# Kernel tuning notes

Measured on AMD Instinct MI355X. Metric: run time of the kernel, lower is better.

## Reference

```python
import jax, jax.numpy as jnp
import numpy as np

BINS = 64
VMIN, VMAX = 0.0, 1.0


def _calc_histogram(x):
    # x: [B, C, H, W] float
    B, C, H, W = x.shape
    x_norm = jnp.clip((x - VMIN) / (VMAX - VMIN), 0.0, 1.0)
    flat = x_norm.reshape(B * C, H * W)
    # torch.histc semantics over [0,1]: bin i = [i/BINS, (i+1)/BINS), last bin closed.
    idx = jnp.clip((flat * BINS).astype(jnp.int32), 0, BINS - 1)  # [B*C, HW]
    row_offset = (jnp.arange(B * C, dtype=jnp.int32) * BINS)[:, None]
    flat_idx = (idx + row_offset).reshape(-1)
    counts = jax.ops.segment_sum(
        jnp.ones(flat_idx.shape, dtype=x.dtype), flat_idx,
        num_segments=B * C * BINS,
    ).reshape(B * C, BINS)
    counts = counts / jnp.clip(counts.sum(axis=1, keepdims=True), 1e-8, None)
    return counts.reshape(B, C, BINS)


def reference(fake_images, real_images):
    hist_fake = _calc_histogram(fake_images)
    hist_real = _calc_histogram(real_images)
    # loss_type == 'l1'
    return jnp.abs(hist_fake - hist_real).mean()


def setup_inputs() -> dict:
    key = jax.random.key(0)
    k1, k2 = jax.random.split(key)
    shape = (32, 3, 512, 512)
    fake_images = jax.random.uniform(k1, shape, dtype=jnp.float32)
    real_images = jax.random.uniform(k2, shape, dtype=jnp.float32)
    return {"fake_images": fake_images, "real_images": real_images}
```

## Files before the change

kernel.cpp:

```cpp
#include <hip/hip_runtime.h>
#include <hip/hip_bf16.h>


#define HW        262144
#define ROWS      96
#define NBINS     64
#define BPR       8
#define CHUNK     (HW / BPR)
#define THREADS   256
#define F4_ITERS  (CHUNK / 4 / THREADS)
#define NBLOCKS   (2 * ROWS * BPR)
#define NREG      64
#define PITCH     65
#define PRIV_W    (NREG * PITCH)

__global__ __launch_bounds__(THREADS)
void hist_kernel(const float* __restrict__ fake,
                 const float* __restrict__ real,
                 unsigned int* __restrict__ partial) {
    __shared__ unsigned int priv[PRIV_W];
    __shared__ unsigned int comb[4][NBINS];

    const int tid  = threadIdx.x;
    const int lane = tid & 63;
    const int wv   = tid >> 6;

    for (int k = tid; k < PRIV_W; k += THREADS) priv[k] = 0u;
    __syncthreads();

    const int b     = blockIdx.x;
    const int chunk = b & (BPR - 1);
    const int rowg  = b >> 3;
    const float* src = (rowg < ROWS) ? fake : real;
    const int row    = (rowg < ROWS) ? rowg : (rowg - ROWS);

    const float4* __restrict__ p =
        (const float4*)(src + (size_t)row * HW + (size_t)chunk * CHUNK);

    unsigned int* __restrict__ reg = &priv[(tid >> 2) * PITCH];

#pragma unroll 4
    for (int i = 0; i < F4_ITERS; ++i) {
        float4 v = p[i * THREADS + tid];
        int b0 = min((int)(v.x * 64.0f), 63);
        int b1 = min((int)(v.y * 64.0f), 63);
        int b2 = min((int)(v.z * 64.0f), 63);
        int b3 = min((int)(v.w * 64.0f), 63);
        atomicAdd(&reg[b0], 1u);
        atomicAdd(&reg[b1], 1u);
        atomicAdd(&reg[b2], 1u);
        atomicAdd(&reg[b3], 1u);
    }
    __syncthreads();

    unsigned cnt = 0;
#pragma unroll
    for (int r = 0; r < 16; ++r)
        cnt += priv[(wv * 16 + r) * PITCH + lane];
    comb[wv][lane] = cnt;
    __syncthreads();

    if (tid < NBINS) {
        unsigned s = comb[0][tid] + comb[1][tid] + comb[2][tid] + comb[3][tid];
        partial[(size_t)b * NBINS + tid] = s;
    }
}

__global__ __launch_bounds__(1024)
void loss_kernel(const unsigned int* __restrict__ partial,
                 float* __restrict__ out) {
    const int tid = threadIdx.x;
    int acc = 0;
#pragma unroll
    for (int q = 0; q < 6; ++q) {
        const int pIdx = q * 1024 + tid;
        const int r  = pIdx >> 6;
        const int bb = pIdx & 63;
        unsigned cf = 0, cr = 0;
#pragma unroll
        for (int c = 0; c < BPR; ++c) {
            cf += partial[((r * BPR + c) * NBINS) + bb];
            cr += partial[(((ROWS + r) * BPR + c) * NBINS) + bb];
        }
        int d = (int)cf - (int)cr;
        acc += (d < 0) ? -d : d;
    }
#pragma unroll
    for (int off = 32; off > 0; off >>= 1)
        acc += __shfl_down(acc, off, 64);
    __shared__ int wsum[16];
    if ((tid & 63) == 0) wsum[tid >> 6] = acc;
    __syncthreads();
    if (tid == 0) {
        long long total = 0;
#pragma unroll
        for (int k = 0; k < 16; ++k) total += wsum[k];
        out[0] = (float)((double)total / (262144.0 * 6144.0));
    }
}

extern "C" void kernel_launch(void* const* d_in, const int* in_sizes, int n_in,
                              void* d_out, int out_size, void* d_ws, size_t ws_size,
                              hipStream_t stream) {
    const float* fake = (const float*)d_in[0];
    const float* real = (const float*)d_in[1];
    unsigned int* partial = (unsigned int*)d_ws;
    float* out = (float*)d_out;

    hist_kernel<<<NBLOCKS, THREADS, 0, stream>>>(fake, real, partial);
    loss_kernel<<<1, 1024, 0, stream>>>(partial, out);
}
```

Baseline: 219.4 us.

## Replace LDS atomic histogram with register-packed nibble counters

Replaces per-element LDS atomics on a privatized shared histogram with per-thread register counters that pack 64 bins as 4-bit nibbles across eight 32-bit words. Every 12 elements the nibbles are flushed into byte-wide accumulators, split into low and high halves, and finally transposed through shared memory and summed per bin. This removes LDS atomic contention and traffic from the inner loop, at the cost of many more VALU ops per element, since each element's update is applied to all eight words via selects. Nibble and byte overflow bounds depend on the exact flush cadence and the per-thread element count of 128.

```diff
diff --git a/kernel.cpp b/kernel.cpp
--- a/kernel.cpp
+++ b/kernel.cpp
@@ -10,23 +10,41 @@
 #define THREADS   256
 #define F4_ITERS  (CHUNK / 4 / THREADS)
 #define NBLOCKS   (2 * ROWS * BPR)
-#define NREG      64
-#define PITCH     65
-#define PRIV_W    (NREG * PITCH)
+#define TP        260
+
+__device__ __forceinline__ void bump(unsigned c[8], float x) {
+    int bin = min((int)(x * 64.0f), 63);
+    unsigned long long inc = 1ull << ((unsigned)(bin << 2) & 63u);
+    unsigned lo = (unsigned)inc;
+    unsigned hi = (unsigned)(inc >> 32);
+    int sel = bin >> 4;
+#pragma unroll
+    for (int k = 0; k < 4; ++k) {
+        bool m = (sel == k);
+        c[2 * k]     += m ? lo : 0u;
+        c[2 * k + 1] += m ? hi : 0u;
+    }
+}
+
+__device__ __forceinline__ void flushc(unsigned c[8], unsigned aLo[8], unsigned aHi[8]) {
+#pragma unroll
+    for (int r = 0; r < 8; ++r) {
+        aLo[r] += c[r] & 0x0F0F0F0Fu;
+        aHi[r] += (c[r] >> 4) & 0x0F0F0F0Fu;
+        c[r] = 0u;
+    }
+}
 
 __global__ __launch_bounds__(THREADS)
 void hist_kernel(const float* __restrict__ fake,
                  const float* __restrict__ real,
                  unsigned int* __restrict__ partial) {
-    __shared__ unsigned int priv[PRIV_W];
+    __shared__ unsigned int trbuf[16 * TP];
     __shared__ unsigned int comb[4][NBINS];
 
     const int tid  = threadIdx.x;
     const int lane = tid & 63;
     const int wv   = tid >> 6;
-
-    for (int k = tid; k < PRIV_W; k += THREADS) priv[k] = 0u;
-    __syncthreads();
 
     const int b     = blockIdx.x;
     const int chunk = b & (BPR - 1);
@@ -37,26 +55,43 @@
     const float4* __restrict__ p =
         (const float4*)(src + (size_t)row * HW + (size_t)chunk * CHUNK);
 
-    unsigned int* __restrict__ reg = &priv[(tid >> 2) * PITCH];
+    unsigned c[8]   = {0, 0, 0, 0, 0, 0, 0, 0};
+    unsigned aLo[8] = {0, 0, 0, 0, 0, 0, 0, 0};
+    unsigned aHi[8] = {0, 0, 0, 0, 0, 0, 0, 0};
 
-#pragma unroll 4
-    for (int i = 0; i < F4_ITERS; ++i) {
-        float4 v = p[i * THREADS + tid];
-        int b0 = min((int)(v.x * 64.0f), 63);
-        int b1 = min((int)(v.y * 64.0f), 63);
-        int b2 = min((int)(v.z * 64.0f), 63);
-        int b3 = min((int)(v.w * 64.0f), 63);
-        atomicAdd(&reg[b0], 1u);
-        atomicAdd(&reg[b1], 1u);
-        atomicAdd(&reg[b2], 1u);
-        atomicAdd(&reg[b3], 1u);
+#pragma unroll 1
+    for (int g = 0; g < 10; ++g) {
+#pragma unroll
+        for (int j = 0; j < 3; ++j) {
+            float4 v = p[(g * 3 + j) * THREADS + tid];
+            bump(c, v.x); bump(c, v.y); bump(c, v.z); bump(c, v.w);
+        }
+        flushc(c, aLo, aHi);
     }
+#pragma unroll
+    for (int j = 30; j < 32; ++j) {
+        float4 v = p[j * THREADS + tid];
+        bump(c, v.x); bump(c, v.y); bump(c, v.z); bump(c, v.w);
+    }
+    flushc(c, aLo, aHi);
+
+#pragma unroll
+    for (int w = 0; w < 8; ++w) trbuf[w * TP + tid] = aLo[w];
+#pragma unroll
+    for (int w = 0; w < 8; ++w) trbuf[(w + 8) * TP + tid] = aHi[w];
     __syncthreads();
 
+    const int w  = (lane >> 3) | ((lane & 1) << 3);
+    const int sh = ((lane >> 1) & 3) * 8;
     unsigned cnt = 0;
 #pragma unroll
-    for (int r = 0; r < 16; ++r)
-        cnt += priv[(wv * 16 + r) * PITCH + lane];
+    for (int t4 = 0; t4 < 16; ++t4) {
+        const uint4 q = *(const uint4*)&trbuf[w * TP + wv * 64 + t4 * 4];
+        cnt += (q.x >> sh) & 0xFFu;
+        cnt += (q.y >> sh) & 0xFFu;
+        cnt += (q.z >> sh) & 0xFFu;
+        cnt += (q.w >> sh) & 0xFFu;
+    }
     comb[wv][lane] = cnt;
     __syncthreads();
 
```

Result: no change. 223.0 us (+1.6%).
